# Performance work log

Hardware: AMD Instinct MI355X
Metric: run time of the kernel (lower is better)

## Reference

```python
import jax, jax.numpy as jnp
import numpy as np

B, C, H, W = 2, 32, 128, 128
P = 32                      # encoder patch size (== decoder_out_feat_size_final_linear -> empty up_tail)
D = 512                     # encoder dim == decoder dim (enc_to_dec = Identity)
HEADS, DHEAD = 8, 64
ENC_DEPTH = 4
FLIN, CUP = 32, 4
DI, DS, K, DTR, OUTCH = 32, 8, 4, 2, 20   # SS2D dims (c_in=32 hardcoded in module)


def _ln(x, g, b):
    m = x.mean(-1, keepdims=True)
    v = ((x - m) ** 2).mean(-1, keepdims=True)
    return (x - m) / jnp.sqrt(v + 1e-5) * g + b


def _attn(x, g, b, wqkv, wo, bo):
    Bb, N, _ = x.shape
    qkv = _ln(x, g, b) @ wqkv
    q, k, v = jnp.split(qkv, 3, axis=-1)
    sp = lambda t: t.reshape(Bb, N, HEADS, DHEAD).transpose(0, 2, 1, 3)
    q, k, v = sp(q), sp(k), sp(v)
    a = jax.nn.softmax(jnp.einsum('bhnd,bhmd->bhnm', q, k) * (DHEAD ** -0.5), axis=-1)
    o = jnp.einsum('bhnm,bhmd->bhnd', a, v).transpose(0, 2, 1, 3).reshape(Bb, N, HEADS * DHEAD)
    return o @ wo + bo


def _ff(x, g, b, w1, b1, w2, b2):
    return jax.nn.gelu(_ln(x, g, b) @ w1 + b1, approximate=False) @ w2 + b2


def _conv(x, w, b, groups=1):
    y = jax.lax.conv_general_dilated(x, w, (1, 1), 'SAME',
        dimension_numbers=('NCHW', 'OIHW', 'NCHW'), feature_group_count=groups)
    return y + b[None, :, None, None]


def _fft2c(x):
    x = jnp.fft.ifftshift(x, axes=(-2, -1))
    x = jnp.fft.fft2(x, axes=(-2, -1), norm='ortho')
    return jnp.fft.fftshift(x, axes=(-2, -1))


def _ifft2c(x):
    x = jnp.fft.ifftshift(x, axes=(-2, -1))
    x = jnp.fft.ifft2(x, axes=(-2, -1), norm='ortho')
    return jnp.fft.fftshift(x, axes=(-2, -1))


def setup_inputs():
    key = jax.random.key(0)
    it = iter(jax.random.split(key, 80))
    nk = lambda: next(it)
    rn = lambda shape, s=0.02: jax.random.normal(nk(), shape, jnp.float32) * s
    nh, nw = H // P, W // P
    N = nh * nw
    pd = P * P * C
    inp = {}
    inp['in_imgs'] = jax.random.normal(nk(), (B, C, H, W), jnp.float32)
    inp['in_ksp'] = rn((B, C, H, W), 0.01)
    inp['mask'] = (jax.random.uniform(nk(), (B, 1, H, W)) < 0.3).astype(jnp.float32)
    s = jax.random.normal(nk(), (B, C, H, W), jnp.float32)
    sc = s[:, 0::2] + 1j * s[:, 1::2]
    sc = sc / jnp.sqrt(jnp.sum(jnp.abs(sc) ** 2, axis=1, keepdims=True) + 1e-8)
    inp['sens'] = jnp.stack([sc.real, sc.imag], axis=2).reshape(B, C, H, W)
    # patch embedding: LayerNorm(pd) -> Linear(pd, D) -> LayerNorm(D)
    inp['pe_ln1_g'] = jnp.ones((pd,)); inp['pe_ln1_b'] = jnp.zeros((pd,))
    inp['pe_w'] = rn((pd, D)); inp['pe_b'] = jnp.zeros((D,))
    inp['pe_ln2_g'] = jnp.ones((D,)); inp['pe_ln2_b'] = jnp.zeros((D,))
    inp['pos_emb'] = rn((1, N, D))
    dep = ENC_DEPTH
    inp['enc_aln_g'] = jnp.ones((dep, D)); inp['enc_aln_b'] = jnp.zeros((dep, D))
    inp['enc_wqkv'] = rn((dep, D, 3 * HEADS * DHEAD)); inp['enc_wo'] = rn((dep, HEADS * DHEAD, D)); inp['enc_bo'] = jnp.zeros((dep, D))
    inp['enc_fln_g'] = jnp.ones((dep, D)); inp['enc_fln_b'] = jnp.zeros((dep, D))
    inp['enc_w1'] = rn((dep, D, 2048)); inp['enc_b1'] = jnp.zeros((dep, 2048))
    inp['enc_w2'] = rn((dep, 2048, D)); inp['enc_b2'] = jnp.zeros((dep, D))
    inp['enc_ng'] = jnp.ones((D,)); inp['enc_nb'] = jnp.zeros((D,))
    inp['dec_pos'] = rn((N, D))
    inp['dec_aln_g'] = jnp.ones((D,)); inp['dec_aln_b'] = jnp.zeros((D,))
    inp['dec_wqkv'] = rn((D, 3 * HEADS * DHEAD)); inp['dec_wo'] = rn((HEADS * DHEAD, D)); inp['dec_bo'] = jnp.zeros((D,))
    inp['dec_fln_g'] = jnp.ones((D,)); inp['dec_fln_b'] = jnp.zeros((D,))
    inp['dec_w1'] = rn((D, 3072)); inp['dec_b1'] = jnp.zeros((3072,))
    inp['dec_w2'] = rn((3072, D)); inp['dec_b2'] = jnp.zeros((D,))
    inp['dec_ng'] = jnp.ones((D,)); inp['dec_nb'] = jnp.zeros((D,))
    inp['fin_w'] = rn((D, CUP * FLIN * FLIN)); inp['fin_b'] = jnp.zeros((CUP * FLIN * FLIN,))
    # SS2D params
    inp['ss_in_w'] = rn((C, 2 * DI), 0.1); inp['ss_in_b'] = jnp.zeros((2 * DI,))
    inp['ss_conv_w'] = rn((DI, 1, 3, 3), 0.1); inp['ss_conv_b'] = jnp.zeros((DI,))
    inp['ss_xproj'] = rn((K, DI, DTR + 2 * DS), 0.1)
    inp['ss_dt_w'] = rn((K, DTR, DI), 0.5); inp['ss_dt_b'] = rn((K, DI), 0.1)
    inp['ss_Alog'] = jnp.log(jnp.tile(jnp.arange(1, DS + 1, dtype=jnp.float32), (K, DI, 1)))
    inp['ss_D'] = jnp.ones((K, DI))
    inp['ss_ln_g'] = jnp.ones((DI,)); inp['ss_ln_b'] = jnp.zeros((DI,))
    inp['ss_out_w'] = rn((DI, OUTCH), 0.1); inp['ss_out_b'] = jnp.zeros((OUTCH,))
    # RefinementBlock (in_ch = CUP + 32 + OUTCH = 56)
    inp['last_head_w'] = rn((64, CUP + C + OUTCH, 3, 3), 0.05); inp['last_head_b'] = jnp.zeros((64,))
    inp['res_w1'] = rn((3, 64, 64, 3, 3), 0.05); inp['res_b1'] = jnp.zeros((3, 64))
    inp['res_w2'] = rn((3, 64, 64, 3, 3), 0.05); inp['res_b2'] = jnp.zeros((3, 64))
    inp['last_tail_w'] = rn((2, 64, 3, 3), 0.05); inp['last_tail_b'] = jnp.zeros((2,))
    inp['dc_alpha'] = jnp.array(1.0, jnp.float32)
    return inp


def _forward(in_imgs, in_ksp, mask, sens, pe_ln1_g, pe_ln1_b, pe_w, pe_b, pe_ln2_g, pe_ln2_b, pos_emb, enc_aln_g, enc_aln_b, enc_wqkv, enc_wo, enc_bo, enc_fln_g, enc_fln_b, enc_w1, enc_b1, enc_w2, enc_b2, enc_ng, enc_nb, dec_pos, dec_aln_g, dec_aln_b, dec_wqkv, dec_wo, dec_bo, dec_fln_g, dec_fln_b, dec_w1, dec_b1, dec_w2, dec_b2, dec_ng, dec_nb, fin_w, fin_b, ss_in_w, ss_in_b, ss_conv_w, ss_conv_b, ss_xproj, ss_dt_w, ss_dt_b, ss_Alog, ss_D, ss_ln_g, ss_ln_b, ss_out_w, ss_out_b, last_head_w, last_head_b, res_w1, res_b1, res_w2, res_b2, last_tail_w, last_tail_b, dc_alpha):
    nh, nw = H // P, W // P
    N = nh * nw
    # patchify: bb cc (h p1) (w p2) -> bb (h w) (p1 p2 cc)
    pch = in_imgs.reshape(B, C, nh, P, nw, P).transpose(0, 2, 4, 3, 5, 1).reshape(B, N, P * P * C)
    t = _ln(pch, pe_ln1_g, pe_ln1_b) @ pe_w + pe_b
    t = _ln(t, pe_ln2_g, pe_ln2_b)
    t = t + pos_emb   # pool == 'mean'
    for i in range(ENC_DEPTH):
        t = _attn(t, enc_aln_g[i], enc_aln_b[i], enc_wqkv[i], enc_wo[i], enc_bo[i]) + t
        t = _ff(t, enc_fln_g[i], enc_fln_b[i], enc_w1[i], enc_b1[i], enc_w2[i], enc_b2[i]) + t
    t = _ln(t, enc_ng, enc_nb)
    # decoder transformer (depth 1); enc_to_dec is Identity
    d = t + dec_pos[None]
    d = _attn(d, dec_aln_g, dec_aln_b, dec_wqkv, dec_wo, dec_bo) + d
    d = _ff(d, dec_fln_g, dec_fln_b, dec_w1, dec_b1, dec_w2, dec_b2) + d
    d = _ln(d, dec_ng, dec_nb)
    lat = d @ fin_w + fin_b
    # bb (nh nw) (cc p1 p2) -> bb cc (nh p1) (nw p2); up_tail is empty (P == FLIN)
    x = lat.reshape(B, nh, nw, CUP, FLIN, FLIN).transpose(0, 3, 1, 4, 2, 5).reshape(B, CUP, H, W)
    # ---- SS2D: 4-directional selective scan over in_ksp ----
    L = H * W
    xz = jnp.einsum('bchw,ce->behw', in_ksp, ss_in_w) + ss_in_b[None, :, None, None]
    xs0, z = xz[:, :DI], xz[:, DI:]
    xs0 = jax.nn.silu(_conv(xs0, ss_conv_w, ss_conv_b, groups=DI))
    x_hw = xs0.reshape(B, DI, L)
    x_wh = xs0.transpose(0, 1, 3, 2).reshape(B, DI, L)
    xs = jnp.stack([x_hw, x_wh, x_hw[..., ::-1], x_wh[..., ::-1]], axis=1)   # (B,K,DI,L)
    dbl = jnp.einsum('bkdl,kdc->bkcl', xs, ss_xproj)
    dtr, Bm, Cm = dbl[:, :, :DTR], dbl[:, :, DTR:DTR + DS], dbl[:, :, DTR + DS:]
    dts = jax.nn.softplus(jnp.einsum('bkrl,krd->bkdl', dtr, ss_dt_w) + ss_dt_b[None, :, :, None])
    A = -jnp.exp(ss_Alog)
    a = jnp.exp(jnp.einsum('bkdl,kds->bklds', dts, A))         # transition per step
    bb = jnp.einsum('bkdl,bksl->bklds', dts * xs, Bm)          # input per step
    def comb(e1, e2):
        a1, b1 = e1; a2, b2 = e2
        return a1 * a2, a2 * b1 + b2
    _, hs = jax.lax.associative_scan(comb, (a, bb), axis=2)    # (B,K,L,DI,DS)
    ys = jnp.einsum('bklds,bksl->bkdl', hs, Cm) + ss_D[None, :, :, None] * xs
    yh = ys[:, 0] + ys[:, 2, :, ::-1]
    yw = ys[:, 1] + ys[:, 3, :, ::-1]
    y = yh + yw.reshape(B, DI, W, H).transpose(0, 1, 3, 2).reshape(B, DI, L)
    y = y.reshape(B, DI, H, W).transpose(0, 2, 3, 1)           # BHWC
    y = _ln(y, ss_ln_g, ss_ln_b) * jax.nn.silu(z.transpose(0, 2, 3, 1))
    out_ss = (y @ ss_out_w + ss_out_b).transpose(0, 3, 1, 2)   # (B,OUTCH,H,W)
    # ---- refinement ----
    lrelu = lambda v: jnp.where(v > 0, v, 0.2 * v)
    xc = jnp.concatenate([x, in_imgs, out_ss], axis=1)
    h0 = lrelu(_conv(xc, last_head_w, last_head_b))
    for i in range(3):
        h0 = lrelu(h0 + _conv(lrelu(_conv(h0, res_w1[i], res_b1[i])), res_w2[i], res_b2[i]))
    x_ri = _conv(h0, last_tail_w, last_tail_b)   # (B,2,H,W)
    # ---- data consistency ----
    x_c = (x_ri[:, 0] + 1j * x_ri[:, 1])[:, None]
    k_meas = (in_ksp[:, 0::2] + 1j * in_ksp[:, 1::2]) * 100.0   # k_scale_ratio
    s_c = sens[:, 0::2] + 1j * sens[:, 1::2]
    k_pred = _fft2c(s_c * x_c)
    k_dc = k_pred + mask * dc_alpha * (k_meas - k_pred)
    x_comb = jnp.sum(_ifft2c(k_dc) * jnp.conj(s_c), axis=1)
    out_ri = jnp.stack([x_comb.real, x_comb.imag], axis=1)
    return jnp.sqrt(out_ri[:, 0:1] ** 2 + out_ri[:, 1:2] ** 2 + 1e-12)


reference = _forward
```

## Files before the change

kernel.cpp:

```cpp
#include <hip/hip_runtime.h>

#define PI_F 3.14159265358979323846f

constexpr int L_ = 16384;
constexpr int PD_ = 32768;

__device__ __forceinline__ float sigmoidf_(float x){ return 1.f/(1.f+__expf(-x)); }
__device__ __forceinline__ float softplusf_(float x){ return x>20.f ? x : log1pf(__expf(x)); }
__device__ __forceinline__ float geluf_(float x){ return 0.5f*x*(1.f+erff(x*0.70710678118654752f)); }

__device__ __forceinline__ float2 block_reduce2(float s, float ss){
  __shared__ float r1[256], r2[256];
  int tid = threadIdx.x;
  r1[tid]=s; r2[tid]=ss; __syncthreads();
  for(int o=128;o>0;o>>=1){ if(tid<o){ r1[tid]+=r1[tid+o]; r2[tid]+=r2[tid+o]; } __syncthreads(); }
  float2 out; out.x=r1[0]; out.y=r2[0]; __syncthreads();
  return out;
}

__global__ __launch_bounds__(256) void k_ln_pe(const float* __restrict__ img, const float* __restrict__ g,
                                               const float* __restrict__ bv, float* __restrict__ xn){
  int m = blockIdx.x; int b = m>>4, n = m&15, ih = n>>2, iw = n&3;
  int tid = threadIdx.x;
  const float* base = img + (size_t)b*32*L_;
  float s=0.f, ss=0.f;
  for (int j=tid; j<PD_; j+=256){
    int c=j>>10, p1=(j>>5)&31, p2=j&31;
    float v = base[(size_t)c*L_ + (ih*32+p1)*128 + iw*32+p2];
    s+=v; ss+=v*v;
  }
  float2 r = block_reduce2(s,ss);
  float mean = r.x/(float)PD_;
  float var  = r.y/(float)PD_ - mean*mean;
  float inv = 1.f/sqrtf(var+1e-5f);
  for (int j=tid; j<PD_; j+=256){
    int c=j>>10, p1=(j>>5)&31, p2=j&31;
    float v = base[(size_t)c*L_ + (ih*32+p1)*128 + iw*32+p2];
    int k = (p1*32+p2)*32 + c;
    xn[(size_t)m*PD_ + k] = (v-mean)*inv*g[k] + bv[k];
  }
}

template<int KC, int MODE>
__global__ __launch_bounds__(256) void k_gemm_sk(const float* __restrict__ A, const float* __restrict__ Bw,
                                                 const float* __restrict__ bias, float* __restrict__ C,
                                                 int N, int K){
  __shared__ float As[32][KC];
  int tid=threadIdx.x, tx=tid&63, ty=tid>>6;
  int n = blockIdx.x*64+tx;
  int k0 = blockIdx.y*KC;
  for (int i=tid;i<32*KC;i+=256){
    int r=i/KC, c=i%KC;
    float v=A[(size_t)r*K + k0 + c];
    if (MODE==1) v=geluf_(v);
    As[r][c]=v;
  }
  __syncthreads();
  float acc[8]={0,0,0,0,0,0,0,0};
  for (int kk=0;kk<KC;kk+=4){
    float b0=Bw[(size_t)(k0+kk)*N+n],   b1=Bw[(size_t)(k0+kk+1)*N+n];
    float b2=Bw[(size_t)(k0+kk+2)*N+n], b3=Bw[(size_t)(k0+kk+3)*N+n];
    #pragma unroll
    for (int r=0;r<8;r++){
      const float4 a=*(const float4*)&As[ty*8+r][kk];
      acc[r]+=a.x*b0+a.y*b1+a.z*b2+a.w*b3;
    }
  }
  bool addb = (bias!=nullptr) && (blockIdx.y==0);
  #pragma unroll
  for (int r=0;r<8;r++){
    int m=ty*8+r;
    float v=acc[r]+(addb?bias[n]:0.f);
// ... 109 lines not shown
  int tid=threadIdx.x, tx=tid&31, ty=tid>>5;
  const float* s=src+(size_t)z*L_;
  float* d=dst+(size_t)z*L_;
  for (int r=ty;r<32;r+=8) tile[r][tx]=s[(h0+r)*128+w0+tx];
  __syncthreads();
  for (int r=ty;r<32;r+=8) d[(w0+r)*128+h0+tx]=tile[tx][r];
}

__global__ __launch_bounds__(256) void k_dbl(const float* __restrict__ xs0, const float* __restrict__ xs0T,
                                             const float* __restrict__ xproj, float* __restrict__ dbl){
  int bk=blockIdx.y; int b=bk>>2, k=bk&3;
  int l0=blockIdx.x*256, tid=threadIdx.x;
  const float* src=(k&1)?xs0T:xs0;
  __shared__ float xv[32][256];
  __shared__ float xp[576];
  for (int i=tid;i<576;i+=256) xp[i]=xproj[k*576+i];
  for (int i=tid;i<8192;i+=256){
    int dd=i>>8, p=i&255; int l=l0+p; int li=(k<2)?l:(16383-l);
    xv[dd][p]=src[(size_t)(b*32+dd)*L_+li];
  }
  __syncthreads();
  float xr[32];
  #pragma unroll
  for (int dd=0;dd<32;dd++) xr[dd]=xv[dd][tid];
  float* out=&dbl[((size_t)(b*4+k)*L_ + l0+tid)*18];
  for (int c=0;c<18;c++){
    float a=0.f;
    #pragma unroll
    for (int dd=0;dd<32;dd++) a+=xr[dd]*xp[dd*18+c];
    out[c]=a;
  }
}

__global__ __launch_bounds__(256) void k_scan(const float* __restrict__ dbl, const float* __restrict__ xs0,
                                              const float* __restrict__ xs0T, const float* __restrict__ dtw,
                                              const float* __restrict__ dtb, const float* __restrict__ Alog,
                                              const float* __restrict__ Dp, float* __restrict__ ys){
  int id=blockIdx.x; int d=id&31, k=(id>>5)&3, b=id>>7;
  const float* src=(k&1)?xs0T:xs0;
  bool rev=(k>=2);
  const float* dbase=dbl + (size_t)(b*4+k)*L_*18;
  const float* xbase=src + (size_t)(b*32+d)*L_;
  float w0=dtw[(k*2+0)*32+d], w1=dtw[(k*2+1)*32+d], bb=dtb[k*32+d];
  float Av[8];
  #pragma unroll
  for (int s=0;s<8;s++) Av[s]=-__expf(Alog[(k*32+d)*8+s]);
  float Dv=Dp[k*32+d];
  int t=threadIdx.x, l0=t*64;
  float P[8],Q[8];
  #pragma unroll
  for (int s=0;s<8;s++){P[s]=1.f;Q[s]=0.f;}
  for (int j=0;j<64;j++){
    int l=l0+j;
    const float* e=dbase+(size_t)l*18;
    float dt=softplusf_(e[0]*w0+e[1]*w1+bb);
    float xsv=xbase[rev?(16383-l):l];
    float u=dt*xsv;
    #pragma unroll
    for (int s=0;s<8;s++){
      float a=__expf(dt*Av[s]);
      Q[s]=a*Q[s]+u*e[2+s];
      P[s]*=a;
    }
  }
  __shared__ float Ps[8][256], Qs[8][256];
  #pragma unroll
  for (int s=0;s<8;s++){Ps[s][t]=P[s];Qs[s][t]=Q[s];}
  __syncthreads();
  for (int off=1;off<256;off<<=1){
    float nP[8],nQ[8];
    if (t>=off){
      #pragma unroll
      for (int s=0;s<8;s++){
        float pP=Ps[s][t-off],pQ=Qs[s][t-off];
        nP[s]=pP*Ps[s][t];
        nQ[s]=Ps[s][t]*pQ+Qs[s][t];
      }
    }
    __syncthreads();
    if (t>=off){
      #pragma unroll
      for (int s=0;s<8;s++){Ps[s][t]=nP[s];Qs[s][t]=nQ[s];}
    }
    __syncthreads();
  }
  float hh[8];
  #pragma unroll
  for (int s=0;s<8;s++) hh[s]=(t==0)?0.f:Qs[s][t-1];
  float* yout=&ys[((size_t)(b*4+k)*32+d)*L_];
  for (int j=0;j<64;j++){
    int l=l0+j;
    const float* e=dbase+(size_t)l*18;
    float dt=softplusf_(e[0]*w0+e[1]*w1+bb);
    float xsv=xbase[rev?(16383-l):l];
    float u=dt*xsv;
    float y=0.f;
    #pragma unroll
    for (int s=0;s<8;s++){
      float a=__expf(dt*Av[s]);
      hh[s]=a*hh[s]+u*e[2+s];
      y+=hh[s]*e[10+s];
    }
    yout[l]=y+Dv*xsv;
  }
}

__global__ __launch_bounds__(256) void k_ycomb(const float* __restrict__ ys, const float* __restrict__ xz,
                                               const float* __restrict__ g, const float* __restrict__ bv,
                                               const float* __restrict__ ow, const float* __restrict__ ob,
                                               float* __restrict__ oss){
  int blk=blockIdx.x; int b=blk>>6; int p=(blk&63)*256+threadIdx.x;
  int h=p>>7, w=p&127; int lt=w*128+h;
  __shared__ float lw[640]; __shared__ float lb[20]; __shared__ float lg[32], lbv[32];
  int tid=threadIdx.x;
  for (int i=tid;i<640;i+=256) lw[i]=ow[i];
  if (tid<20) lb[tid]=ob[tid];
  if (tid<32){ lg[tid]=g[tid]; lbv[tid]=bv[tid]; }
  __syncthreads();
  size_t base=(size_t)b*4*32*L_;
  float y[32];
  float s=0.f, ss=0.f;
  #pragma unroll
  for (int d=0;d<32;d++){
    float v=ys[base+(size_t)(0*32+d)*L_+p] + ys[base+(size_t)(2*32+d)*L_+16383-p]
          + ys[base+(size_t)(1*32+d)*L_+lt] + ys[base+(size_t)(3*32+d)*L_+16383-lt];
    y[d]=v; s+=v; ss+=v*v;
  }
  float mean=s/32.f, var=ss/32.f-mean*mean, inv=1.f/sqrtf(var+1e-5f);
  #pragma unroll
  for (int d=0;d<32;d++){
    float yn=(y[d]-mean)*inv*lg[d]+lbv[d];
    float zv=xz[(size_t)(b*64+32+d)*L_+p];
    y[d]=yn*(zv*sigmoidf_(zv));
  }
  for (int c=0;c<20;c++){
    float a=lb[c];
// ... 62 lines not shown
      acc[co][1]+=iv[0][1]*w0+iv[0][2]*w1+iv[0][3]*w2
                 +iv[1][1]*w3+iv[1][2]*w4+iv[1][3]*w5
                 +iv[2][1]*w6+iv[2][2]*w7+iv[2][3]*w8;
      acc[co][2]+=iv[1][0]*w0+iv[1][1]*w1+iv[1][2]*w2
                 +iv[2][0]*w3+iv[2][1]*w4+iv[2][2]*w5
                 +iv[3][0]*w6+iv[3][1]*w7+iv[3][2]*w8;
      acc[co][3]+=iv[1][1]*w0+iv[1][2]*w1+iv[1][3]*w2
                 +iv[2][1]*w3+iv[2][2]*w4+iv[2][3]*w5
                 +iv[3][1]*w6+iv[3][2]*w7+iv[3][3]*w8;
    }
    __syncthreads();
  }
  #pragma unroll
  for (int co=0;co<NCO;co++){
    int gco=cg*NCO+co;
    float* dst=sc+((size_t)((ks*2+b)*Cout+gco))*L_+(size_t)(th0+tr)*128+tw0+tc;
    float2 a={acc[co][0],acc[co][1]}, c={acc[co][2],acc[co][3]};
    *(float2*)dst=a;
    *(float2*)(dst+128)=c;
  }
}

__global__ void k_epi(const float* __restrict__ sc, const float* __restrict__ bias,
                      const float* __restrict__ res, float* __restrict__ out, int Cout, int act){
  int i=blockIdx.x*256+threadIdx.x;
  int co=(i/L_)%Cout;
  size_t half=(size_t)2*Cout*L_;
  float v=sc[i]+sc[half+i]+bias[co];
  if (res) v+=res[i];
  if (act) v=v>0.f?v:0.2f*v;
  out[i]=v;
}

template<int NCO>
__global__ __launch_bounds__(256) void k_conv3(const float* __restrict__ in, const float* __restrict__ wt,
                                               const float* __restrict__ bs, const float* __restrict__ add,
                                               float* __restrict__ out, int Cin, int Cout, int cg_count, int act){
  int b=blockIdx.z/cg_count, cg=blockIdx.z%cg_count;
  int tid=threadIdx.x, tx=tid&15, ty=tid>>4;
  int h=blockIdx.y*16+ty, w=blockIdx.x*16+tx;
  __shared__ float tile[18][18];
  float acc[NCO];
  #pragma unroll
  for (int co=0;co<NCO;co++) acc[co]=0.f;
  for (int ci=0;ci<Cin;ci++){
    const float* src=in+(size_t)(b*Cin+ci)*L_;
    for (int i=tid;i<324;i+=256){
      int r=i/18, c=i%18;
      int gh=blockIdx.y*16+r-1, gw=blockIdx.x*16+c-1;
      tile[r][c]=(gh>=0&&gh<128&&gw>=0&&gw<128)?src[gh*128+gw]:0.f;
    }
    __syncthreads();
    float n0=tile[ty][tx],  n1=tile[ty][tx+1],  n2=tile[ty][tx+2];
    float n3=tile[ty+1][tx],n4=tile[ty+1][tx+1],n5=tile[ty+1][tx+2];
    float n6=tile[ty+2][tx],n7=tile[ty+2][tx+1],n8=tile[ty+2][tx+2];
    const float* wp=wt+((size_t)(cg*NCO)*Cin+ci)*9;
    #pragma unroll
    for (int co=0;co<NCO;co++){
      const float* wq=wp+(size_t)co*Cin*9;
      acc[co]+=n0*wq[0]+n1*wq[1]+n2*wq[2]+n3*wq[3]+n4*wq[4]+n5*wq[5]+n6*wq[6]+n7*wq[7]+n8*wq[8];
    }
    __syncthreads();
  }
  #pragma unroll
  for (int co=0;co<NCO;co++){
    int gco=cg*NCO+co;
    float v=acc[co]+bs[gco];
    if (add) v+=add[(size_t)(b*Cout+gco)*L_+h*128+w];
    if (act) v=v>0.f?v:0.2f*v;
    out[(size_t)(b*Cout+gco)*L_+h*128+w]=v;
  }
}

__device__ __forceinline__ int rev7(int x){
  return ((x&1)<<6)|((x&2)<<4)|((x&4)<<2)|(x&8)|((x&16)>>2)|((x&32)>>4)|((x&64)>>6);
}

__global__ __launch_bounds__(256) void k_fft_dc(const float* __restrict__ x_ri, const float* __restrict__ sens,
                                                const float* __restrict__ ksp, const float* __restrict__ mask,
                                                const float* __restrict__ alpha_p, float* __restrict__ acc){
  int blk=blockIdx.x; int b=blk>>4, coil=blk&15;
  __shared__ float Sr[16384];
  __shared__ float Si[16384];
  __shared__ float twr[64], twi[64];
  int tid=threadIdx.x;
  if (tid<64){ float ang=-2.f*PI_F*(float)tid/128.f; twr[tid]=cosf(ang); twi[tid]=sinf(ang); }
  const float* srp=sens+(size_t)(b*32+2*coil)*L_;
  const float* sip=sens+(size_t)(b*32+2*coil+1)*L_;
  const float* xrp=x_ri+(size_t)(b*2)*L_;
  const float* xip=xrp+L_;
  for (int i=tid;i<16384;i+=256){
    int h=i>>7,w=i&127;
    float sg=((h+w)&1)?-1.f:1.f;
    float sr=srp[i],si=sip[i],xr=xrp[i],xi=xip[i];
    Sr[i]=sg*(sr*xr-si*xi);
    Si[i]=sg*(sr*xi+si*xr);
  }
  __syncthreads();
  for (int s=0;s<7;s++){
    int m=64>>s;
    for (int q=tid;q<8192;q+=256){
      int row=q>>6, jj=q&63;
      int j=jj&(m-1), gg=jj>>(6-s);
      int kpos=(gg<<(7-s))+j;
      int i0=row*128+kpos, i1=i0+m;
      int tw=j<<s;
      float ur=Sr[i0],ui=Si[i0],vr=Sr[i1],vi=Si[i1];
      Sr[i0]=ur+vr; Si[i0]=ui+vi;
      float dr=ur-vr,di=ui-vi,wr=twr[tw],wi=twi[tw];
      Sr[i1]=dr*wr-di*wi; Si[i1]=dr*wi+di*wr;
    }
    __syncthreads();
  }
  for (int s=0;s<7;s++){
    int m=64>>s;
    for (int q=tid;q<8192;q+=256){
      int cpos=q&127, jj=q>>7;
      int j=jj&(m-1), gg=jj>>(6-s);
      int kpos=(gg<<(7-s))+j;
      int i0=kpos*128+cpos, i1=i0+m*128;
      int tw=j<<s;
      float ur=Sr[i0],ui=Si[i0],vr=Sr[i1],vi=Si[i1];
      Sr[i0]=ur+vr; Si[i0]=ui+vi;
      float dr=ur-vr,di=ui-vi,wr=twr[tw],wi=twi[tw];
      Sr[i1]=dr*wr-di*wi; Si[i1]=dr*wi+di*wr;
    }
    __syncthreads();
  }
  float alpha=alpha_p[0];
  const float* krp=ksp+(size_t)(b*32+2*coil)*L_;
  const float* kip=ksp+(size_t)(b*32+2*coil+1)*L_;
  const float* mkp=mask+(size_t)b*L_;
  for (int i=tid;i<16384;i+=256){
    int i1=i>>7, i2=i&127;
    int k1=rev7(i1), k2=rev7(i2);
    int kidx=k1*128+k2;
    float mv=mkp[kidx]*alpha;
    float sg=((k1+k2)&1)?-128.f:128.f;
    float kr=krp[kidx]*100.f*sg, ki=kip[kidx]*100.f*sg;
    Sr[i]=(1.f-mv)*Sr[i]+mv*kr;
    Si[i]=(1.f-mv)*Si[i]+mv*ki;
  }
  __syncthreads();
  for (int s=0;s<7;s++){
    int m=1<<s;
    for (int q=tid;q<8192;q+=256){
      int cpos=q&127, jj=q>>7;
      int j=jj&(m-1), gg=jj>>s;
      int kpos=(gg<<(s+1))+j;
      int i0=kpos*128+cpos, i1=i0+m*128;
      int tw=j<<(6-s);
      float wr=twr[tw], wi=-twi[tw];
      float vr=Sr[i1],vi=Si[i1];
      float tr=vr*wr-vi*wi, ti=vr*wi+vi*wr;
      float ur=Sr[i0],ui=Si[i0];
      Sr[i0]=ur+tr; Si[i0]=ui+ti;
      Sr[i1]=ur-tr; Si[i1]=ui-ti;
    }
    __syncthreads();
  }
  for (int s=0;s<7;s++){
    int m=1<<s;
    for (int q=tid;q<8192;q+=256){
      int row=q>>6, jj=q&63;
      int j=jj&(m-1), gg=jj>>s;
      int kpos=(gg<<(s+1))+j;
      int i0=row*128+kpos, i1=i0+m;
      int tw=j<<(6-s);
      float wr=twr[tw], wi=-twi[tw];
      float vr=Sr[i1],vi=Si[i1];
      float tr=vr*wr-vi*wi, ti=vr*wi+vi*wr;
      float ur=Sr[i0],ui=Si[i0];
      Sr[i0]=ur+tr; Si[i0]=ui+ti;
      Sr[i1]=ur-tr; Si[i1]=ui-ti;
    }
    __syncthreads();
  }
  float* accr=acc+(size_t)(b*2)*L_;
  float* acci=accr+L_;
  for (int i=tid;i<16384;i+=256){
    int h=i>>7,w=i&127;
    float sc=(((h+w)&1)?-1.f:1.f)*(1.f/16384.f);
    float wr2=Sr[i]*sc, wi2=Si[i]*sc;
    float sr=srp[i], si=sip[i];
    atomicAdd(&accr[i], sr*wr2+si*wi2);
    atomicAdd(&acci[i], sr*wi2-si*wr2);
  }
}

__global__ void k_mag(const float* __restrict__ acc, float* __restrict__ out){
  int i=blockIdx.x*256+threadIdx.x;
  int b=i>>14, p=i&16383;
  float re=acc[(size_t)(b*2)*L_+p], im=acc[(size_t)(b*2+1)*L_+p];
  out[i]=sqrtf(re*re+im*im+1e-12f);
}

extern "C" void kernel_launch(void* const* d_in, const int* in_sizes, int n_in,
                              void* d_out, int out_size, void* d_ws, size_t ws_size,
                              hipStream_t stream){
  const float* in_imgs=(const float*)d_in[0];
  const float* in_ksp=(const float*)d_in[1];
  const float* mask=(const float*)d_in[2];
  const float* sens=(const float*)d_in[3];
  const float* pe_ln1_g=(const float*)d_in[4];
  const float* pe_ln1_b=(const float*)d_in[5];
  const float* pe_w=(const float*)d_in[6];
  const float* pe_b=(const float*)d_in[7];
  const float* pe_ln2_g=(const float*)d_in[8];
  const float* pe_ln2_b=(const float*)d_in[9];
  const float* pos_emb=(const float*)d_in[10];
  const float* enc_aln_g=(const float*)d_in[11];
  const float* enc_aln_b=(const float*)d_in[12];
  const float* enc_wqkv=(const float*)d_in[13];
  const float* enc_wo=(const float*)d_in[14];
  const float* enc_bo=(const float*)d_in[15];
  const float* enc_fln_g=(const float*)d_in[16];
  const float* enc_fln_b=(const float*)d_in[17];
  const float* enc_w1=(const float*)d_in[18];
  const float* enc_b1=(const float*)d_in[19];
// ... 14 lines not shown
  const float* dec_w2=(const float*)d_in[34];
  const float* dec_b2=(const float*)d_in[35];
  const float* dec_ng=(const float*)d_in[36];
  const float* dec_nb=(const float*)d_in[37];
  const float* fin_w=(const float*)d_in[38];
  const float* fin_b=(const float*)d_in[39];
  const float* ss_in_w=(const float*)d_in[40];
  const float* ss_in_b=(const float*)d_in[41];
  const float* ss_conv_w=(const float*)d_in[42];
  const float* ss_conv_b=(const float*)d_in[43];
  const float* ss_xproj=(const float*)d_in[44];
  const float* ss_dt_w=(const float*)d_in[45];
  const float* ss_dt_b=(const float*)d_in[46];
  const float* ss_Alog=(const float*)d_in[47];
  const float* ss_D=(const float*)d_in[48];
  const float* ss_ln_g=(const float*)d_in[49];
  const float* ss_ln_b=(const float*)d_in[50];
  const float* ss_out_w=(const float*)d_in[51];
  const float* ss_out_b=(const float*)d_in[52];
  const float* head_w=(const float*)d_in[53];
  const float* head_b=(const float*)d_in[54];
  const float* res_w1=(const float*)d_in[55];
  const float* res_b1=(const float*)d_in[56];
  const float* res_w2=(const float*)d_in[57];
  const float* res_b2=(const float*)d_in[58];
  const float* tail_w=(const float*)d_in[59];
  const float* tail_b=(const float*)d_in[60];
  const float* dc_alpha=(const float*)d_in[61];

  char* ws=(char*)d_ws;
  size_t off=0;
  auto alloc=[&](size_t nfloats)->float*{ float* p=(float*)(ws+off); off+=((nfloats*4+255)/256)*256; return p; };
  float* xn   =alloc((size_t)32*32768);
  float* tA   =alloc(32*512);
  float* tB   =alloc(32*512);
  float* aln  =alloc(32*512);
  float* qkv  =alloc(32*1536);
  float* attno=alloc(32*512);
  float* ffh  =alloc(32*3072);
  float* xup  =alloc((size_t)2*4*L_);
  float* xz   =alloc((size_t)2*64*L_);
  float* xs0  =alloc((size_t)2*32*L_);
  float* xs0T =alloc((size_t)2*32*L_);
  float* dbl  =alloc((size_t)2*4*L_*18);
  float* ys   =alloc((size_t)2*4*32*L_);
  float* oss  =alloc((size_t)2*20*L_);
  float* xc   =alloc((size_t)2*56*L_);
  float* h0   =alloc((size_t)2*64*L_);
  float* tmpc =alloc((size_t)2*64*L_);
  float* csc  =alloc((size_t)2*2*64*L_);
  float* x_ri =alloc((size_t)2*2*L_);
  float* accb =alloc((size_t)2*2*L_);
  (void)ws_size; (void)in_sizes; (void)n_in; (void)out_size;

  k_ln_pe<<<32,256,0,stream>>>(in_imgs, pe_ln1_g, pe_ln1_b, xn);
  hipMemsetAsync(tA, 0, 32*512*4, stream);
  k_gemm_sk<256,0><<<dim3(8,128),256,0,stream>>>(xn, pe_w, pe_b, tA, 512, 32768);
  k_pe_post<<<32,256,0,stream>>>(tA, pe_ln2_g, pe_ln2_b, pos_emb);

  for (int i=0;i<4;i++){
    k_ln_tok<<<32,256,0,stream>>>(tA, enc_aln_g+i*512, enc_aln_b+i*512, aln);
    hipMemsetAsync(qkv, 0, 32*1536*4, stream);
    k_gemm_sk<64,0><<<dim3(24,8),256,0,stream>>>(aln, enc_wqkv+(size_t)i*512*1536, nullptr, qkv, 1536, 512);
    k_attn<<<16,256,0,stream>>>(qkv, attno);
    k_gemm_sk<64,0><<<dim3(8,8),256,0,stream>>>(attno, enc_wo+(size_t)i*512*512, enc_bo+i*512, tA, 512, 512);
    k_ln_tok<<<32,256,0,stream>>>(tA, enc_fln_g+i*512, enc_fln_b+i*512, aln);
    hipMemsetAsync(ffh, 0, 32*2048*4, stream);
    k_gemm_sk<64,0><<<dim3(32,8),256,0,stream>>>(aln, enc_w1+(size_t)i*512*2048, enc_b1+i*2048, ffh, 2048, 512);
    k_gemm_sk<64,1><<<dim3(8,32),256,0,stream>>>(ffh, enc_w2+(size_t)i*2048*512, enc_b2+i*512, tA, 512, 2048);
  }
  k_ln_tok<<<32,256,0,stream>>>(tA, enc_ng, enc_nb, tA);
  k_addpos<<<64,256,0,stream>>>(tA, dec_pos, tB);
  k_ln_tok<<<32,256,0,stream>>>(tB, dec_aln_g, dec_aln_b, aln);
  hipMemsetAsync(qkv, 0, 32*1536*4, stream);
  k_gemm_sk<64,0><<<dim3(24,8),256,0,stream>>>(aln, dec_wqkv, nullptr, qkv, 1536, 512);
  k_attn<<<16,256,0,stream>>>(qkv, attno);
  k_gemm_sk<64,0><<<dim3(8,8),256,0,stream>>>(attno, dec_wo, dec_bo, tB, 512, 512);
  k_ln_tok<<<32,256,0,stream>>>(tB, dec_fln_g, dec_fln_b, aln);
  hipMemsetAsync(ffh, 0, 32*3072*4, stream);
  k_gemm_sk<64,0><<<dim3(48,8),256,0,stream>>>(aln, dec_w1, dec_b1, ffh, 3072, 512);
  k_gemm_sk<64,1><<<dim3(8,48),256,0,stream>>>(ffh, dec_w2, dec_b2, tB, 512, 3072);
  k_ln_tok<<<32,256,0,stream>>>(tB, dec_ng, dec_nb, tB);
  hipMemsetAsync(xup, 0, (size_t)2*4*L_*4, stream);
  k_gemm_sk<64,2><<<dim3(64,8),256,0,stream>>>(tB, fin_w, fin_b, xup, 4096, 512);

  k_xz<<<128,256,0,stream>>>(in_ksp, ss_in_w, ss_in_b, xz);
  k_dwconv<<<4096,256,0,stream>>>(xz, ss_conv_w, ss_conv_b, xs0);
  k_transpose<<<dim3(4,4,64),256,0,stream>>>(xs0, xs0T);
  k_dbl<<<dim3(64,8),256,0,stream>>>(xs0, xs0T, ss_xproj, dbl);
  k_scan<<<256,256,0,stream>>>(dbl, xs0, xs0T, ss_dt_w, ss_dt_b, ss_Alog, ss_D, ys);
  k_ycomb<<<128,256,0,stream>>>(ys, xz, ss_ln_g, ss_ln_b, ss_out_w, ss_out_b, oss);

  k_concat<<<7168,256,0,stream>>>(xup, in_imgs, oss, xc);
  k_conv3s<4><<<dim3(16,16,4),256,0,stream>>>(xc, head_w, csc, 56, 64, 28);
  k_epi<<<8192,256,0,stream>>>(csc, head_b, nullptr, h0, 64, 1);
  for (int i=0;i<3;i++){
    k_conv3s<4><<<dim3(16,16,4),256,0,stream>>>(h0, res_w1+(size_t)i*64*64*9, csc, 64, 64, 32);
    k_epi<<<8192,256,0,stream>>>(csc, res_b1+i*64, nullptr, tmpc, 64, 1);
    k_conv3s<4><<<dim3(16,16,4),256,0,stream>>>(tmpc, res_w2+(size_t)i*64*64*9, csc, 64, 64, 32);
    k_epi<<<8192,256,0,stream>>>(csc, res_b2+i*64, h0, h0, 64, 1);
  }
  k_conv3<2><<<dim3(8,8,2),256,0,stream>>>(h0, tail_w, tail_b, nullptr, x_ri, 64, 2, 1, 0);

  hipMemsetAsync(accb, 0, (size_t)2*2*L_*4, stream);
  k_fft_dc<<<32,256,0,stream>>>(x_ri, sens, in_ksp, mask, dc_alpha, accb);
  k_mag<<<128,256,0,stream>>>(accb, (float*)d_out);
}
```

Measured before the change: 1.841 ms.

## Split patch-embed LN, selective scan, tail conv and FFT-DC into more parallel kernels

Splits the patch-embedding LayerNorm into a partial-sum kernel with atomic statistics and a separate normalize kernel, so it runs on many more blocks. Restructures the selective scan into chunked three-phase form: per-chunk state products, a sequential prefix over chunks, then a rescan. Each thread in the scan handles one state dimension, with shuffle reductions and shared-memory staging. It also routes the tail conv through the split-K conv plus epilogue, and breaks the per-coil 2D FFT data-consistency kernel into row, column and row passes over a global scratch buffer. The aim is to fix very low block counts (32 or 256 blocks). The cost is extra launches and global round-trips for the intermediates.

```diff
diff --git a/kernel.cpp b/kernel.cpp
--- a/kernel.cpp
+++ b/kernel.cpp
@@ -18,26 +18,38 @@
   return out;
 }
 
-__global__ __launch_bounds__(256) void k_ln_pe(const float* __restrict__ img, const float* __restrict__ g,
-                                               const float* __restrict__ bv, float* __restrict__ xn){
-  int m = blockIdx.x; int b = m>>4, n = m&15, ih = n>>2, iw = n&3;
-  int tid = threadIdx.x;
-  const float* base = img + (size_t)b*32*L_;
+__global__ __launch_bounds__(256) void k_pesum(const float* __restrict__ img, float* __restrict__ stats){
+  int blk=blockIdx.x; int m=blk>>3, sl=blk&7;
+  int b=m>>4, n=m&15, ih=n>>2, iw=n&3;
+  int tid=threadIdx.x;
+  const float* base=img+(size_t)b*32*L_;
   float s=0.f, ss=0.f;
-  for (int j=tid; j<PD_; j+=256){
+  for (int i=tid;i<4096;i+=256){
+    int j=sl*4096+i;
     int c=j>>10, p1=(j>>5)&31, p2=j&31;
-    float v = base[(size_t)c*L_ + (ih*32+p1)*128 + iw*32+p2];
+    float v=base[(size_t)c*L_+(ih*32+p1)*128+iw*32+p2];
     s+=v; ss+=v*v;
   }
-  float2 r = block_reduce2(s,ss);
-  float mean = r.x/(float)PD_;
-  float var  = r.y/(float)PD_ - mean*mean;
-  float inv = 1.f/sqrtf(var+1e-5f);
-  for (int j=tid; j<PD_; j+=256){
+  float2 r=block_reduce2(s,ss);
+  if (tid==0){ atomicAdd(&stats[m*2],r.x); atomicAdd(&stats[m*2+1],r.y); }
+}
+
+__global__ __launch_bounds__(256) void k_penorm(const float* __restrict__ img, const float* __restrict__ stats,
+                                                const float* __restrict__ g, const float* __restrict__ bv,
+                                                float* __restrict__ xn){
+  int blk=blockIdx.x; int m=blk>>3, sl=blk&7;
+  int b=m>>4, n=m&15, ih=n>>2, iw=n&3;
+  int tid=threadIdx.x;
+  const float* base=img+(size_t)b*32*L_;
+  float mean=stats[m*2]/(float)PD_;
+  float var =stats[m*2+1]/(float)PD_-mean*mean;
+  float inv =1.f/sqrtf(var+1e-5f);
+  for (int i=tid;i<4096;i+=256){
+    int j=sl*4096+i;
     int c=j>>10, p1=(j>>5)&31, p2=j&31;
-    float v = base[(size_t)c*L_ + (ih*32+p1)*128 + iw*32+p2];
-    int k = (p1*32+p2)*32 + c;
-    xn[(size_t)m*PD_ + k] = (v-mean)*inv*g[k] + bv[k];
+    float v=base[(size_t)c*L_+(ih*32+p1)*128+iw*32+p2];
+    int k=(p1*32+p2)*32+c;
+    xn[(size_t)m*PD_+k]=(v-mean)*inv*g[k]+bv[k];
   }
 }
 
@@ -213,76 +225,89 @@
   }
 }
 
-__global__ __launch_bounds__(256) void k_scan(const float* __restrict__ dbl, const float* __restrict__ xs0,
-                                              const float* __restrict__ xs0T, const float* __restrict__ dtw,
-                                              const float* __restrict__ dtb, const float* __restrict__ Alog,
-                                              const float* __restrict__ Dp, float* __restrict__ ys){
-  int id=blockIdx.x; int d=id&31, k=(id>>5)&3, b=id>>7;
+__global__ __launch_bounds__(256) void k_scan1(const float* __restrict__ dbl, const float* __restrict__ xs0,
+                                               const float* __restrict__ xs0T, const float* __restrict__ dtw,
+                                               const float* __restrict__ dtb, const float* __restrict__ Alog,
+                                               float2* __restrict__ sm){
+  int blk=blockIdx.x; int bk=blk>>7, c=blk&127;
+  int b=bk>>2, k=bk&3;
+  int tid=threadIdx.x, d=tid>>3, s=tid&7;
+  __shared__ float ed[128][18];
+  __shared__ float xsl[32][128];
+  const float* dbase=dbl+((size_t)bk*L_+c*128)*18;
+  for (int i=tid;i<2304;i+=256) ((float*)ed)[i]=dbase[i];
   const float* src=(k&1)?xs0T:xs0;
   bool rev=(k>=2);
-  const float* dbase=dbl + (size_t)(b*4+k)*L_*18;
-  const float* xbase=src + (size_t)(b*32+d)*L_;
+  for (int i=tid;i<4096;i+=256){
+    int dd=i>>7, j=i&127; int l=c*128+j;
+    xsl[dd][j]=src[(size_t)(b*32+dd)*L_+(rev?(16383-l):l)];
+  }
+  __syncthreads();
   float w0=dtw[(k*2+0)*32+d], w1=dtw[(k*2+1)*32+d], bb=dtb[k*32+d];
-  float Av[8];
-  #pragma unroll
-  for (int s=0;s<8;s++) Av[s]=-__expf(Alog[(k*32+d)*8+s]);
+  float Av=-__expf(Alog[(k*32+d)*8+s]);
+  float P=1.f, Q=0.f;
+  for (int j=0;j<128;j++){
+    float dt=softplusf_(ed[j][0]*w0+ed[j][1]*w1+bb);
+    float u=dt*xsl[d][j];
+    float a=__expf(dt*Av);
+    Q=a*Q+u*ed[j][2+s];
+    P*=a;
+  }
+  sm[((size_t)bk*128+c)*256+tid]=make_float2(P,Q);
+}
+
+__global__ __launch_bounds__(256) void k_scan2(const float2* __restrict__ sm, float* __restrict__ pre){
+  int bk=blockIdx.x, tid=threadIdx.x;
+  float run=0.f;
+  for (int c=0;c<128;c++){
+    size_t idx=((size_t)bk*128+c)*256+tid;
+    pre[idx]=run;
+    float2 pq=sm[idx];
+    run=pq.x*run+pq.y;
+  }
+}
+
+__global__ __launch_bounds__(256) void k_scan3(const float* __restrict__ dbl, const float* __restrict__ xs0,
+                                               const float* __restrict__ xs0T, const float* __restrict__ dtw,
+                                               const float* __restrict__ dtb, const float* __restrict__ Alog,
+                                               const float* __restrict__ Dp, const float* __restrict__ pre,
+                                               float* __restrict__ ys){
+  int blk=blockIdx.x; int bk=blk>>7, c=blk&127;
+  int b=bk>>2, k=bk&3;
+  int tid=threadIdx.x, d=tid>>3, s=tid&7;
+  __shared__ float ed[128][18];
+  __shared__ float xsl[32][128];
+  __shared__ float ybuf[32][128];
+  const float* dbase=dbl+((size_t)bk*L_+c*128)*18;
+  for (int i=tid;i<2304;i+=256) ((float*)ed)[i]=dbase[i];
+  const float* src=(k&1)?xs0T:xs0;
+  bool rev=(k>=2);
+  for (int i=tid;i<4096;i+=256){
+    int dd=i>>7, j=i&127; int l=c*128+j;
+    xsl[dd][j]=src[(size_t)(b*32+dd)*L_+(rev?(16383-l):l)];
+  }
+  __syncthreads();
+  float w0=dtw[(k*2+0)*32+d], w1=dtw[(k*2+1)*32+d], bb=dtb[k*32+d];
+  float Av=-__expf(Alog[(k*32+d)*8+s]);
   float Dv=Dp[k*32+d];
-  int t=threadIdx.x, l0=t*64;
-  float P[8],Q[8];
-  #pragma unroll
-  for (int s=0;s<8;s++){P[s]=1.f;Q[s]=0.f;}
-  for (int j=0;j<64;j++){
-    int l=l0+j;
-    const float* e=dbase+(size_t)l*18;
-    float dt=softplusf_(e[0]*w0+e[1]*w1+bb);
-    float xsv=xbase[rev?(16383-l):l];
+  float h=pre[((size_t)bk*128+c)*256+tid];
+  for (int j=0;j<128;j++){
+    float xsv=xsl[d][j];
+    float dt=softplusf_(ed[j][0]*w0+ed[j][1]*w1+bb);
     float u=dt*xsv;
-    #pragma unroll
-    for (int s=0;s<8;s++){
-      float a=__expf(dt*Av[s]);
-      Q[s]=a*Q[s]+u*e[2+s];
-      P[s]*=a;
-    }
-  }
-  __shared__ float Ps[8][256], Qs[8][256];
-  #pragma unroll
-  for (int s=0;s<8;s++){Ps[s][t]=P[s];Qs[s][t]=Q[s];}
-  __syncthreads();
-  for (int off=1;off<256;off<<=1){
-    float nP[8],nQ[8];
-    if (t>=off){
-      #pragma unroll
-      for (int s=0;s<8;s++){
-        float pP=Ps[s][t-off],pQ=Qs[s][t-off];
-        nP[s]=pP*Ps[s][t];
-        nQ[s]=Ps[s][t]*pQ+Qs[s][t];
-      }
-    }
-    __syncthreads();
-    if (t>=off){
-      #pragma unroll
-      for (int s=0;s<8;s++){Ps[s][t]=nP[s];Qs[s][t]=nQ[s];}
-    }
-    __syncthreads();
-  }
-  float hh[8];
-  #pragma unroll
-  for (int s=0;s<8;s++) hh[s]=(t==0)?0.f:Qs[s][t-1];
-  float* yout=&ys[((size_t)(b*4+k)*32+d)*L_];
-  for (int j=0;j<64;j++){
-    int l=l0+j;
-    const float* e=dbase+(size_t)l*18;
-    float dt=softplusf_(e[0]*w0+e[1]*w1+bb);
-    float xsv=xbase[rev?(16383-l):l];
-    float u=dt*xsv;
-    float y=0.f;
-    #pragma unroll
-    for (int s=0;s<8;s++){
-      float a=__expf(dt*Av[s]);
-      hh[s]=a*hh[s]+u*e[2+s];
-      y+=hh[s]*e[10+s];
-    }
-    yout[l]=y+Dv*xsv;
+    float a=__expf(dt*Av);
+    h=a*h+u*ed[j][2+s];
+    float yp=h*ed[j][10+s];
+    yp+=__shfl_xor(yp,1,8);
+    yp+=__shfl_xor(yp,2,8);
+    yp+=__shfl_xor(yp,4,8);
+    if (s==0) ybuf[d][j]=yp+Dv*xsv;
+  }
+  __syncthreads();
+  float* yout=ys+((size_t)bk*32)*L_+c*128;
+  for (int i=tid;i<4096;i+=256){
+    int dd=i>>7, j=i&127;
+    yout[(size_t)dd*L_+j]=ybuf[dd][j];
   }
 }
 
@@ -411,56 +436,15 @@
   out[i]=v;
 }
 
-template<int NCO>
-__global__ __launch_bounds__(256) void k_conv3(const float* __restrict__ in, const float* __restrict__ wt,
-                                               const float* __restrict__ bs, const float* __restrict__ add,
-                                               float* __restrict__ out, int Cin, int Cout, int cg_count, int act){
-  int b=blockIdx.z/cg_count, cg=blockIdx.z%cg_count;
-  int tid=threadIdx.x, tx=tid&15, ty=tid>>4;
-  int h=blockIdx.y*16+ty, w=blockIdx.x*16+tx;
-  __shared__ float tile[18][18];
-  float acc[NCO];
-  #pragma unroll
-  for (int co=0;co<NCO;co++) acc[co]=0.f;
-  for (int ci=0;ci<Cin;ci++){
-    const float* src=in+(size_t)(b*Cin+ci)*L_;
-    for (int i=tid;i<324;i+=256){
-      int r=i/18, c=i%18;
-      int gh=blockIdx.y*16+r-1, gw=blockIdx.x*16+c-1;
-      tile[r][c]=(gh>=0&&gh<128&&gw>=0&&gw<128)?src[gh*128+gw]:0.f;
-    }
-    __syncthreads();
-    float n0=tile[ty][tx],  n1=tile[ty][tx+1],  n2=tile[ty][tx+2];
-    float n3=tile[ty+1][tx],n4=tile[ty+1][tx+1],n5=tile[ty+1][tx+2];
-    float n6=tile[ty+2][tx],n7=tile[ty+2][tx+1],n8=tile[ty+2][tx+2];
-    const float* wp=wt+((size_t)(cg*NCO)*Cin+ci)*9;
-    #pragma unroll
-    for (int co=0;co<NCO;co++){
-      const float* wq=wp+(size_t)co*Cin*9;
-      acc[co]+=n0*wq[0]+n1*wq[1]+n2*wq[2]+n3*wq[3]+n4*wq[4]+n5*wq[5]+n6*wq[6]+n7*wq[7]+n8*wq[8];
-    }
-    __syncthreads();
-  }
-  #pragma unroll
-  for (int co=0;co<NCO;co++){
-    int gco=cg*NCO+co;
-    float v=acc[co]+bs[gco];
-    if (add) v+=add[(size_t)(b*Cout+gco)*L_+h*128+w];
-    if (act) v=v>0.f?v:0.2f*v;
-    out[(size_t)(b*Cout+gco)*L_+h*128+w]=v;
-  }
-}
-
 __device__ __forceinline__ int rev7(int x){
   return ((x&1)<<6)|((x&2)<<4)|((x&4)<<2)|(x&8)|((x&16)>>2)|((x&32)>>4)|((x&64)>>6);
 }
 
-__global__ __launch_bounds__(256) void k_fft_dc(const float* __restrict__ x_ri, const float* __restrict__ sens,
-                                                const float* __restrict__ ksp, const float* __restrict__ mask,
-                                                const float* __restrict__ alpha_p, float* __restrict__ acc){
-  int blk=blockIdx.x; int b=blk>>4, coil=blk&15;
-  __shared__ float Sr[16384];
-  __shared__ float Si[16384];
+__global__ __launch_bounds__(256) void k_fftA(const float* __restrict__ x_ri, const float* __restrict__ sens,
+                                              float* __restrict__ tmp){
+  int blk=blockIdx.x; int b=blk>>7, coil=(blk>>3)&15, rg=blk&7;
+  int r0=rg*16;
+  __shared__ float Ar[16][128], Ai[16][128];
   __shared__ float twr[64], twi[64];
   int tid=threadIdx.x;
   if (tid<64){ float ang=-2.f*PI_F*(float)tid/128.f; twr[tid]=cosf(ang); twi[tid]=sinf(ang); }
@@ -468,41 +452,62 @@
   const float* sip=sens+(size_t)(b*32+2*coil+1)*L_;
   const float* xrp=x_ri+(size_t)(b*2)*L_;
   const float* xip=xrp+L_;
-  for (int i=tid;i<16384;i+=256){
-    int h=i>>7,w=i&127;
-    float sg=((h+w)&1)?-1.f:1.f;
-    float sr=srp[i],si=sip[i],xr=xrp[i],xi=xip[i];
-    Sr[i]=sg*(sr*xr-si*xi);
-    Si[i]=sg*(sr*xi+si*xr);
+  for (int i=tid;i<2048;i+=256){
+    int lr=i>>7, w=i&127; int gh=r0+lr; int idx=gh*128+w;
+    float sg=((gh+w)&1)?-1.f:1.f;
+    float sr=srp[idx],si=sip[idx],xr=xrp[idx],xi=xip[idx];
+    Ar[lr][w]=sg*(sr*xr-si*xi);
+    Ai[lr][w]=sg*(sr*xi+si*xr);
   }
   __syncthreads();
   for (int s=0;s<7;s++){
     int m=64>>s;
-    for (int q=tid;q<8192;q+=256){
-      int row=q>>6, jj=q&63;
+    for (int q=tid;q<1024;q+=256){
+      int lr=q>>6, jj=q&63;
       int j=jj&(m-1), gg=jj>>(6-s);
       int kpos=(gg<<(7-s))+j;
-      int i0=row*128+kpos, i1=i0+m;
       int tw=j<<s;
-      float ur=Sr[i0],ui=Si[i0],vr=Sr[i1],vi=Si[i1];
-      Sr[i0]=ur+vr; Si[i0]=ui+vi;
+      float ur=Ar[lr][kpos],ui=Ai[lr][kpos],vr=Ar[lr][kpos+m],vi=Ai[lr][kpos+m];
+      Ar[lr][kpos]=ur+vr; Ai[lr][kpos]=ui+vi;
       float dr=ur-vr,di=ui-vi,wr=twr[tw],wi=twi[tw];
-      Sr[i1]=dr*wr-di*wi; Si[i1]=dr*wi+di*wr;
+      Ar[lr][kpos+m]=dr*wr-di*wi; Ai[lr][kpos+m]=dr*wi+di*wr;
     }
     __syncthreads();
   }
+  float* tr=tmp+(size_t)(b*16+coil)*2*L_;
+  float* ti=tr+L_;
+  for (int i=tid;i<2048;i+=256){
+    int lr=i>>7, w=i&127; int idx=(r0+lr)*128+w;
+    tr[idx]=Ar[lr][w]; ti[idx]=Ai[lr][w];
+  }
+}
+
+__global__ __launch_bounds__(256) void k_fftB(float* __restrict__ tmp, const float* __restrict__ ksp,
+                                              const float* __restrict__ mask, const float* __restrict__ alpha_p){
+  int blk=blockIdx.x; int b=blk>>7, coil=(blk>>3)&15, cg=blk&7;
+  int c0=cg*16;
+  __shared__ float Br[128][17], Bi[128][17];
+  __shared__ float twr[64], twi[64];
+  int tid=threadIdx.x;
+  if (tid<64){ float ang=-2.f*PI_F*(float)tid/128.f; twr[tid]=cosf(ang); twi[tid]=sinf(ang); }
+  float* tr=tmp+(size_t)(b*16+coil)*2*L_;
+  float* ti=tr+L_;
+  for (int i=tid;i<2048;i+=256){
+    int r=i>>4, lc=i&15;
+    Br[r][lc]=tr[r*128+c0+lc]; Bi[r][lc]=ti[r*128+c0+lc];
+  }
+  __syncthreads();
   for (int s=0;s<7;s++){
     int m=64>>s;
-    for (int q=tid;q<8192;q+=256){
-      int cpos=q&127, jj=q>>7;
+    for (int q=tid;q<1024;q+=256){
+      int lc=q&15, jj=q>>4;
       int j=jj&(m-1), gg=jj>>(6-s);
       int kpos=(gg<<(7-s))+j;
-      int i0=kpos*128+cpos, i1=i0+m*128;
       int tw=j<<s;
-      float ur=Sr[i0],ui=Si[i0],vr=Sr[i1],vi=Si[i1];
-      Sr[i0]=ur+vr; Si[i0]=ui+vi;
+      float ur=Br[kpos][lc],ui=Bi[kpos][lc],vr=Br[kpos+m][lc],vi=Bi[kpos+m][lc];
+      Br[kpos][lc]=ur+vr; Bi[kpos][lc]=ui+vi;
       float dr=ur-vr,di=ui-vi,wr=twr[tw],wi=twi[tw];
-      Sr[i1]=dr*wr-di*wi; Si[i1]=dr*wi+di*wr;
+      Br[kpos+m][lc]=dr*wr-di*wi; Bi[kpos+m][lc]=dr*wi+di*wr;
     }
     __syncthreads();
   }
@@ -510,60 +515,81 @@
   const float* krp=ksp+(size_t)(b*32+2*coil)*L_;
   const float* kip=ksp+(size_t)(b*32+2*coil+1)*L_;
   const float* mkp=mask+(size_t)b*L_;
-  for (int i=tid;i<16384;i+=256){
-    int i1=i>>7, i2=i&127;
-    int k1=rev7(i1), k2=rev7(i2);
+  for (int i=tid;i<2048;i+=256){
+    int r=i>>4, lc=i&15;
+    int k1=rev7(r), k2=rev7(c0+lc);
     int kidx=k1*128+k2;
     float mv=mkp[kidx]*alpha;
     float sg=((k1+k2)&1)?-128.f:128.f;
     float kr=krp[kidx]*100.f*sg, ki=kip[kidx]*100.f*sg;
-    Sr[i]=(1.f-mv)*Sr[i]+mv*kr;
-    Si[i]=(1.f-mv)*Si[i]+mv*ki;
+    Br[r][lc]=(1.f-mv)*Br[r][lc]+mv*kr;
+    Bi[r][lc]=(1.f-mv)*Bi[r][lc]+mv*ki;
   }
   __syncthreads();
   for (int s=0;s<7;s++){
     int m=1<<s;
-    for (int q=tid;q<8192;q+=256){
-      int cpos=q&127, jj=q>>7;
+    for (int q=tid;q<1024;q+=256){
+      int lc=q&15, jj=q>>4;
       int j=jj&(m-1), gg=jj>>s;
       int kpos=(gg<<(s+1))+j;
-      int i0=kpos*128+cpos, i1=i0+m*128;
       int tw=j<<(6-s);
       float wr=twr[tw], wi=-twi[tw];
-      float vr=Sr[i1],vi=Si[i1];
-      float tr=vr*wr-vi*wi, ti=vr*wi+vi*wr;
-      float ur=Sr[i0],ui=Si[i0];
-      Sr[i0]=ur+tr; Si[i0]=ui+ti;
-      Sr[i1]=ur-tr; Si[i1]=ui-ti;
+      float vr=Br[kpos+m][lc],vi=Bi[kpos+m][lc];
+      float t2r=vr*wr-vi*wi, t2i=vr*wi+vi*wr;
+      float ur=Br[kpos][lc],ui=Bi[kpos][lc];
+      Br[kpos][lc]=ur+t2r; Bi[kpos][lc]=ui+t2i;
+      Br[kpos+m][lc]=ur-t2r; Bi[kpos+m][lc]=ui-t2i;
     }
     __syncthreads();
   }
+  for (int i=tid;i<2048;i+=256){
+    int r=i>>4, lc=i&15;
+    tr[r*128+c0+lc]=Br[r][lc]; ti[r*128+c0+lc]=Bi[r][lc];
+  }
+}
+
+__global__ __launch_bounds__(256) void k_fftC(const float* __restrict__ tmp, const float* __restrict__ sens,
+                                              float* __restrict__ acc){
+  int blk=blockIdx.x; int b=blk>>7, coil=(blk>>3)&15, rg=blk&7;
+  int r0=rg*16;
+  __shared__ float Ar[16][128], Ai[16][128];
+  __shared__ float twr[64], twi[64];
+  int tid=threadIdx.x;
+  if (tid<64){ float ang=-2.f*PI_F*(float)tid/128.f; twr[tid]=cosf(ang); twi[tid]=sinf(ang); }
+  const float* tr=tmp+(size_t)(b*16+coil)*2*L_;
+  const float* ti=tr+L_;
+  for (int i=tid;i<2048;i+=256){
+    int lr=i>>7, w=i&127; int idx=(r0+lr)*128+w;
+    Ar[lr][w]=tr[idx]; Ai[lr][w]=ti[idx];
+  }
+  __syncthreads();
   for (int s=0;s<7;s++){
     int m=1<<s;
-    for (int q=tid;q<8192;q+=256){
-      int row=q>>6, jj=q&63;
+    for (int q=tid;q<1024;q+=256){
+      int lr=q>>6, jj=q&63;
       int j=jj&(m-1), gg=jj>>s;
       int kpos=(gg<<(s+1))+j;
-      int i0=row*128+kpos, i1=i0+m;
       int tw=j<<(6-s);
       float wr=twr[tw], wi=-twi[tw];
-      float vr=Sr[i1],vi=Si[i1];
-      float tr=vr*wr-vi*wi, ti=vr*wi+vi*wr;
-      float ur=Sr[i0],ui=Si[i0];
-      Sr[i0]=ur+tr; Si[i0]=ui+ti;
-      Sr[i1]=ur-tr; Si[i1]=ui-ti;
+      float vr=Ar[lr][kpos+m],vi=Ai[lr][kpos+m];
+      float t2r=vr*wr-vi*wi, t2i=vr*wi+vi*wr;
+      float ur=Ar[lr][kpos],ui=Ai[lr][kpos];
+      Ar[lr][kpos]=ur+t2r; Ai[lr][kpos]=ui+t2i;
+      Ar[lr][kpos+m]=ur-t2r; Ai[lr][kpos+m]=ui-t2i;
     }
     __syncthreads();
   }
+  const float* srp=sens+(size_t)(b*32+2*coil)*L_;
+  const float* sip=sens+(size_t)(b*32+2*coil+1)*L_;
   float* accr=acc+(size_t)(b*2)*L_;
   float* acci=accr+L_;
-  for (int i=tid;i<16384;i+=256){
-    int h=i>>7,w=i&127;
-    float sc=(((h+w)&1)?-1.f:1.f)*(1.f/16384.f);
-    float wr2=Sr[i]*sc, wi2=Si[i]*sc;
-    float sr=srp[i], si=sip[i];
-    atomicAdd(&accr[i], sr*wr2+si*wi2);
-    atomicAdd(&acci[i], sr*wi2-si*wr2);
+  for (int i=tid;i<2048;i+=256){
+    int lr=i>>7, w=i&127; int gh=r0+lr; int idx=gh*128+w;
+    float sc=(((gh+w)&1)?-1.f:1.f)*(1.f/16384.f);
+    float wr2=Ar[lr][w]*sc, wi2=Ai[lr][w]*sc;
+    float sr=srp[idx], si=sip[idx];
+    atomicAdd(&accr[idx], sr*wr2+si*wi2);
+    atomicAdd(&acci[idx], sr*wi2-si*wr2);
   }
 }
 
@@ -644,6 +670,7 @@
   size_t off=0;
   auto alloc=[&](size_t nfloats)->float*{ float* p=(float*)(ws+off); off+=((nfloats*4+255)/256)*256; return p; };
   float* xn   =alloc((size_t)32*32768);
+  float* stats=alloc(64);
   float* tA   =alloc(32*512);
   float* tB   =alloc(32*512);
   float* aln  =alloc(32*512);
@@ -656,16 +683,21 @@
   float* xs0T =alloc((size_t)2*32*L_);
   float* dbl  =alloc((size_t)2*4*L_*18);
   float* ys   =alloc((size_t)2*4*32*L_);
+  float* smv  =alloc((size_t)8*128*256*2);
+  float* prев =alloc((size_t)8*128*256);
   float* oss  =alloc((size_t)2*20*L_);
   float* xc   =alloc((size_t)2*56*L_);
   float* h0   =alloc((size_t)2*64*L_);
   float* tmpc =alloc((size_t)2*64*L_);
   float* csc  =alloc((size_t)2*2*64*L_);
   float* x_ri =alloc((size_t)2*2*L_);
+  float* ftmp =alloc((size_t)32*2*L_);
   float* accb =alloc((size_t)2*2*L_);
   (void)ws_size; (void)in_sizes; (void)n_in; (void)out_size;
 
-  k_ln_pe<<<32,256,0,stream>>>(in_imgs, pe_ln1_g, pe_ln1_b, xn);
+  hipMemsetAsync(stats, 0, 64*4, stream);
+  k_pesum<<<256,256,0,stream>>>(in_imgs, stats);
+  k_penorm<<<256,256,0,stream>>>(in_imgs, stats, pe_ln1_g, pe_ln1_b, xn);
   hipMemsetAsync(tA, 0, 32*512*4, stream);
   k_gemm_sk<256,0><<<dim3(8,128),256,0,stream>>>(xn, pe_w, pe_b, tA, 512, 32768);
   k_pe_post<<<32,256,0,stream>>>(tA, pe_ln2_g, pe_ln2_b, pos_emb);
@@ -700,7 +732,9 @@
   k_dwconv<<<4096,256,0,stream>>>(xz, ss_conv_w, ss_conv_b, xs0);
   k_transpose<<<dim3(4,4,64),256,0,stream>>>(xs0, xs0T);
   k_dbl<<<dim3(64,8),256,0,stream>>>(xs0, xs0T, ss_xproj, dbl);
-  k_scan<<<256,256,0,stream>>>(dbl, xs0, xs0T, ss_dt_w, ss_dt_b, ss_Alog, ss_D, ys);
+  k_scan1<<<1024,256,0,stream>>>(dbl, xs0, xs0T, ss_dt_w, ss_dt_b, ss_Alog, (float2*)smv);
+  k_scan2<<<8,256,0,stream>>>((const float2*)smv, prев);
+  k_scan3<<<1024,256,0,stream>>>(dbl, xs0, xs0T, ss_dt_w, ss_dt_b, ss_Alog, ss_D, prев, ys);
   k_ycomb<<<128,256,0,stream>>>(ys, xz, ss_ln_g, ss_ln_b, ss_out_w, ss_out_b, oss);
 
   k_concat<<<7168,256,0,stream>>>(xup, in_imgs, oss, xc);
@@ -712,9 +746,12 @@
     k_conv3s<4><<<dim3(16,16,4),256,0,stream>>>(tmpc, res_w2+(size_t)i*64*64*9, csc, 64, 64, 32);
     k_epi<<<8192,256,0,stream>>>(csc, res_b2+i*64, h0, h0, 64, 1);
   }
-  k_conv3<2><<<dim3(8,8,2),256,0,stream>>>(h0, tail_w, tail_b, nullptr, x_ri, 64, 2, 1, 0);
+  k_conv3s<2><<<dim3(16,1,4),256,0,stream>>>(h0, tail_w, csc, 64, 2, 32);
+  k_epi<<<256,256,0,stream>>>(csc, tail_b, nullptr, x_ri, 2, 0);
 
   hipMemsetAsync(accb, 0, (size_t)2*2*L_*4, stream);
-  k_fft_dc<<<32,256,0,stream>>>(x_ri, sens, in_ksp, mask, dc_alpha, accb);
+  k_fftA<<<256,256,0,stream>>>(x_ri, sens, ftmp);
+  k_fftB<<<256,256,0,stream>>>(ftmp, in_ksp, mask, dc_alpha);
+  k_fftC<<<256,256,0,stream>>>(ftmp, sens, accb);
   k_mag<<<128,256,0,stream>>>(accb, (float*)d_out);
 }
```

After: 1.792 ms. 2.6% less time.
